# Optimization experiments

Hardware: AMD Instinct MI355X
Metric: run time of the kernel (lower is better)

The kernel has to match this reference:

```python
import jax, jax.numpy as jnp
import numpy as np

D_MODEL = 2048
N_HEADS = 16
N_KV = 4
D_HEAD = D_MODEL // N_HEADS  # 128
KERNEL = 4
TOTAL_QKV = (N_HEADS + 2 * N_KV) * D_HEAD  # 3072
BATCH, SEQ = 2, 2048


def setup_inputs() -> dict:
    key = jax.random.key(0)
    ks = jax.random.split(key, 6)
    s = 1.0 / np.sqrt(D_MODEL)
    return {
        "hidden_states": jax.random.normal(ks[0], (BATCH, SEQ, D_MODEL), jnp.float32),
        "w_q": jax.random.normal(ks[1], (D_MODEL, N_HEADS * D_HEAD), jnp.float32) * s,
        "w_k": jax.random.normal(ks[2], (D_MODEL, N_KV * D_HEAD), jnp.float32) * s,
        "w_v": jax.random.normal(ks[3], (D_MODEL, N_KV * D_HEAD), jnp.float32) * s,
        "w_o": jax.random.normal(ks[4], (N_HEADS * D_HEAD, D_MODEL), jnp.float32) * s,
        "conv_w": jax.random.normal(ks[5], (TOTAL_QKV, KERNEL), jnp.float32) * 0.1,
    }


def _canon_b(x, conv_w):
    """Depthwise causal conv1d with residual. x: [B,S,C], conv_w: [C,K]."""
    K = conv_w.shape[1]
    xp = jnp.pad(x, ((0, 0), (K - 1, 0), (0, 0)))  # left pad for causality
    S = x.shape[1]
    out = sum(xp[:, k:k + S, :] * conv_w[:, k] for k in range(K))
    return x + out


def reference(hidden_states, w_q, w_k, w_v, w_o, conv_w):
    B, S, _ = hidden_states.shape
    q = hidden_states @ w_q   # [B,S,Hq*Dh]
    k = hidden_states @ w_k   # [B,S,Hkv*Dh]
    v = hidden_states @ w_v
    qkv = jnp.concatenate([q, k, v], axis=-1)
    qkv = _canon_b(qkv, conv_w)
    q_dim = N_HEADS * D_HEAD
    kv_dim = N_KV * D_HEAD
    q, k, v = jnp.split(qkv, [q_dim, q_dim + kv_dim], axis=-1)
    q = q.reshape(B, S, N_HEADS, D_HEAD)
    k = k.reshape(B, S, N_KV, D_HEAD)
    v = v.reshape(B, S, N_KV, D_HEAD)
    # GQA: repeat kv heads to match query heads
    groups = N_HEADS // N_KV
    k = jnp.repeat(k, groups, axis=2)
    v = jnp.repeat(v, groups, axis=2)
    scale = 1.0 / np.sqrt(D_HEAD)
    scores = jnp.einsum("bqhd,bkhd->bhqk", q, k) * scale  # [B,H,S,S]
    causal = jnp.tril(jnp.ones((S, S), dtype=bool))
    scores = jnp.where(causal, scores, jnp.finfo(scores.dtype).min)
    probs = jax.nn.softmax(scores, axis=-1)
    attended = jnp.einsum("bhqk,bkhd->bqhd", probs, v)  # [B,S,H,Dh]
    attended = attended.reshape(B, S, N_HEADS * D_HEAD)
    return attended @ w_o
```

## Files before the change

### kernel.cpp

```cpp
#include <hip/hip_runtime.h>
#include <stdint.h>

typedef unsigned short u16;
typedef short short8 __attribute__((ext_vector_type(8)));
typedef float f32x4 __attribute__((ext_vector_type(4)));
typedef float f32x16 __attribute__((ext_vector_type(16)));

#define DM    2048
#define NH    16
#define NKV   4
#define DH    128
#define TQKV  3072
#define NB    2
#define SEQL  2048
#define MROWS (NB * SEQL)
#define QDIM  (NH * DH)
#define KVDIM (NKV * DH)
#define QSCALE 0.08838834764831845f

#define MFMA16(a, b, c) __builtin_amdgcn_mfma_f32_16x16x32_bf16((a), (b), (c), 0, 0, 0)
#define MFMA32(a, b, c) __builtin_amdgcn_mfma_f32_32x32x16_bf16((a), (b), (c), 0, 0, 0)

__device__ __forceinline__ u16 f2bf(float f) {
  uint32_t u = __float_as_uint(f);
  u += 0x7fffu + ((u >> 16) & 1u);
  return (u16)(u >> 16);
}
__device__ __forceinline__ float bf2f(u16 h) {
  return __uint_as_float(((uint32_t)h) << 16);
}
__device__ __forceinline__ void gload16(const u16* g, u16* l) {
  __builtin_amdgcn_global_load_lds((__attribute__((address_space(1))) void*)(u16*)g,
                                   (__attribute__((address_space(3))) void*)l, 16, 0, 0);
}
__device__ __forceinline__ uint32_t cvtpk(float lo, float hi) {
  uint32_t r;
  asm("v_cvt_pk_bf16_f32 %0, %1, %2" : "=v"(r) : "v"(lo), "v"(hi));
  return r;
}
__device__ __forceinline__ void swapln(uint32_t& a, uint32_t& b) {
  asm volatile("v_permlane32_swap_b32 %0, %1" : "+v"(a), "+v"(b));
}

__global__ void k_f32_to_bf16(const float* __restrict__ src, u16* __restrict__ dst, int n) {
  int i = (blockIdx.x * blockDim.x + threadIdx.x) * 4;
  if (i >= n) return;
  float4 v = *reinterpret_cast<const float4*>(src + i);
  u16 o0 = f2bf(v.x), o1 = f2bf(v.y), o2 = f2bf(v.z), o3 = f2bf(v.w);
  u16* d = dst + i;
  d[0] = o0; d[1] = o1; d[2] = o2; d[3] = o3;
}

__global__ void k_transpose_f32_bf16(const float* __restrict__ src, u16* __restrict__ dst,
                                     int K, int N, int rowOff, int dstLd) {
  __shared__ float t[32][33];
  const int n0 = blockIdx.x * 32, k0 = blockIdx.y * 32;
  const int tx = threadIdx.x, ty = threadIdx.y;
#pragma unroll
  for (int i = ty; i < 32; i += 8)
    t[i][tx] = src[(size_t)(k0 + i) * N + (n0 + tx)];
  __syncthreads();
#pragma unroll
  for (int i = ty; i < 32; i += 8)
    dst[(size_t)(rowOff + n0 + i) * dstLd + (k0 + tx)] = f2bf(t[tx][i]);
}

__global__ void k_transpose_bf16(const u16* __restrict__ src, u16* __restrict__ dst, int R, int C) {
  __shared__ u16 t[32][33];
  const size_t zoff = (size_t)blockIdx.z * R * C;
  const int c0 = blockIdx.x * 32, r0 = blockIdx.y * 32;
  const int tx = threadIdx.x, ty = threadIdx.y;
#pragma unroll
  for (int i = ty; i < 32; i += 8)
    t[i][tx] = src[zoff + (size_t)(r0 + i) * C + (c0 + tx)];
  __syncthreads();
#pragma unroll
  for (int i = ty; i < 32; i += 8)
    dst[zoff + (size_t)(c0 + i) * R + (r0 + tx)] = t[tx][i];
}

template <int OUTBF>
__global__ __launch_bounds__(256) void k_gemm_bt(const u16* __restrict__ A, const u16* __restrict__ Bt,
                                                 float* __restrict__ Cf, u16* __restrict__ Cb,
                                                 int M, int N, int K) {
  __shared__ u16 As[2][128 * 32];
  __shared__ u16 Bs[2][128 * 32];
  const int tid = threadIdx.x;
  const int m0 = blockIdx.x * 128;
  const int n0 = blockIdx.y * 128;
  const int r  = tid >> 2;
  const int c8 = (tid & 3) << 3;
  const u16* Ag0 = A  + (size_t)(m0 + r) * K + c8;
  const u16* Ag1 = A  + (size_t)(m0 + 64 + r) * K + c8;
  const u16* Bg0 = Bt + (size_t)(n0 + r) * K + c8;
  const u16* Bg1 = Bt + (size_t)(n0 + 64 + r) * K + c8;

  auto stage = [&](int buf, int kt) {
    const int kg = kt * 32;
    gload16(Ag0 + kg, &As[buf][tid * 8]);
    gload16(Ag1 + kg, &As[buf][2048 + tid * 8]);
    gload16(Bg0 + kg, &Bs[buf][tid * 8]);
    gload16(Bg1 + kg, &Bs[buf][2048 + tid * 8]);
  };

  f32x4 acc[4][4];
#pragma unroll
  for (int i = 0; i < 4; ++i)
#pragma unroll
    for (int j = 0; j < 4; ++j) acc[i][j] = (f32x4){0.f, 0.f, 0.f, 0.f};

  const int wv = tid >> 6, ln = tid & 63;
  const int wr = (wv >> 1) * 64, wc = (wv & 1) * 64;
  const int lr = ln & 15, lko = (ln >> 4) * 8;

  stage(0, 0);
  __syncthreads();

  const int nk = K >> 5;
  for (int kt = 0; kt < nk; ++kt) {
    const int cur = kt & 1;
    if (kt + 1 < nk) stage(cur ^ 1, kt + 1);
    short8 af[4], bf[4];
#pragma unroll
    for (int i = 0; i < 4; ++i)
      af[i] = *reinterpret_cast<const short8*>(&As[cur][(wr + i * 16 + lr) * 32 + lko]);
#pragma unroll
    for (int i = 0; i < 4; ++i)
      bf[i] = *reinterpret_cast<const short8*>(&Bs[cur][(wc + i * 16 + lr) * 32 + lko]);
#pragma unroll
    for (int i = 0; i < 4; ++i)
#pragma unroll
      for (int j = 0; j < 4; ++j)
        acc[i][j] = MFMA16(af[i], bf[j], acc[i][j]);
    __syncthreads();
  }

  const int rg = (ln >> 4) * 4;
#pragma unroll
  for (int i = 0; i < 4; ++i) {
#pragma unroll
    for (int j = 0; j < 4; ++j) {
      const int row = m0 + wr + i * 16 + rg;
      const int col = n0 + wc + j * 16 + lr;
#pragma unroll
      for (int q = 0; q < 4; ++q) {
        float v = acc[i][j][q];
        if (OUTBF) Cb[(size_t)(row + q) * N + col] = f2bf(v);
        else       Cf[(size_t)(row + q) * N + col] = v;
      }
    }
  }
}

__global__ void k_conv_route(const u16* __restrict__ qkv, const float* __restrict__ cw,
                             u16* __restrict__ Qh, u16* __restrict__ Kh, u16* __restrict__ Vsd) {
  const int row = blockIdx.x;
  const int b = row >> 11, s = row & 2047;
  const int c = threadIdx.x * 8;
  float x[4][8];
#pragma unroll
  for (int k = 0; k < 4; ++k) {
    const int sr = s + k - 3;
    if (sr < 0) {
#pragma unroll
      for (int j = 0; j < 8; ++j) x[k][j] = 0.f;
    } else {
      short8 v = *reinterpret_cast<const short8*>(&qkv[(size_t)(b * SEQL + sr) * TQKV + c]);
#pragma unroll
      for (int j = 0; j < 8; ++j) x[k][j] = bf2f((u16)v[j]);
    }
  }
  float o[8];
#pragma unroll
  for (int j = 0; j < 8; ++j) {
    float4 w4 = *reinterpret_cast<const float4*>(&cw[(c + j) * 4]);
    o[j] = x[3][j] + x[0][j] * w4.x + x[1][j] * w4.y + x[2][j] * w4.z + x[3][j] * w4.w;
  }
  short8 ov;
  if (c < QDIM) {
#pragma unroll
    for (int j = 0; j < 8; ++j) ov[j] = (short)f2bf(o[j] * QSCALE);
    const int h = c >> 7, d = c & 127;
    *reinterpret_cast<short8*>(&Qh[((size_t)(b * NH + h) * SEQL + s) * DH + d]) = ov;
  } else if (c < QDIM + KVDIM) {
#pragma unroll
    for (int j = 0; j < 8; ++j) ov[j] = (short)f2bf(o[j]);
    const int cc = c - QDIM;
    const int h = cc >> 7, d = cc & 127;
    *reinterpret_cast<short8*>(&Kh[((size_t)(b * NKV + h) * SEQL + s) * DH + d]) = ov;
  } else {
#pragma unroll
    for (int j = 0; j < 8; ++j) ov[j] = (short)f2bf(o[j]);
    const int cc = c - QDIM - KVDIM;
    const int h = cc >> 7, d = cc & 127;
    *reinterpret_cast<short8*>(&Vsd[((size_t)(b * NKV + h) * SEQL + s) * DH + d]) = ov;
  }
}

__global__ __launch_bounds__(512) void k_attn(const u16* __restrict__ Qh, const u16* __restrict__ Kh,
                                              const u16* __restrict__ Vt, u16* __restrict__ att) {
  __shared__ u16 Ks[2][64 * 128];
  __shared__ u16 Vs[2][128 * 64];
  const int qb = blockIdx.x, h = blockIdx.y, b = blockIdx.z;
  const int kvh = h >> 2;
  const int tid = threadIdx.x, wv = tid >> 6, ln = tid & 63;
  const int lq = ln & 31, hi = ln >> 5;
  const int hi16 = hi * 16;
  const int q0w = qb * 256 + wv * 32;
  const int qg = q0w + lq;
  const int swr = (lq & 7) << 4;

  const u16* qrow = Qh + ((size_t)(b * NH + h) * SEQL + qg) * DH;
  short8 qf[8];
#pragma unroll
  for (int dblk = 0; dblk < 8; ++dblk)
    qf[dblk] = *reinterpret_cast<const short8*>(qrow + dblk * 16 + hi * 8);

  const u16* kg = Kh + (size_t)(b * NKV + kvh) * SEQL * DH;
  const u16* vg = Vt + (size_t)(b * NKV + kvh) * DH * SEQL;

  const int ck0 = tid, ck1 = tid + 512;
  const int krow0 = ck0 >> 4, kcb0 = (ck0 & 15) << 4;
  const int krow1 = ck1 >> 4, kcb1 = (ck1 & 15) << 4;
  const int koff0 = krow0 * DH + ((kcb0 ^ ((krow0 & 7) << 4)) >> 1);
  const int koff1 = krow1 * DH + ((kcb1 ^ ((krow1 & 7) << 4)) >> 1);
  const int vd0 = ck0 >> 3, vcb0 = (ck0 & 7) << 4;
  const int vd1 = ck1 >> 3, vcb1 = (ck1 & 7) << 4;
  const int voff0 = vd0 * SEQL + ((vcb0 ^ ((vd0 & 7) << 4)) >> 1);
  const int voff1 = vd1 * SEQL + ((vcb1 ^ ((vd1 & 7) << 4)) >> 1);

  auto stage = [&](int buf, int kvs) {
    gload16(kg + (size_t)kvs * DH + koff0, &Ks[buf][ck0 * 8]);
    gload16(kg + (size_t)kvs * DH + koff1, &Ks[buf][ck1 * 8]);
    gload16(vg + (size_t)kvs + voff0, &Vs[buf][ck0 * 8]);
    gload16(vg + (size_t)kvs + voff1, &Vs[buf][ck1 * 8]);
  };

  f32x16 oacc[4];
#pragma unroll
  for (int nb = 0; nb < 4; ++nb)
#pragma unroll
    for (int r = 0; r < 16; ++r) oacc[nb][r] = 0.f;
  float mrow = -1e30f, lrow = 0.f;

  const int ntiles = (qb + 1) * 4;
  stage(0, 0);
  __syncthreads();

  for (int t = 0; t < ntiles; ++t) {
    const int cur = t & 1;
    const int kvs = t * 64;
    if (t + 1 < ntiles) stage(cur ^ 1, kvs + 64);
    if (kvs <= q0w + 31) {
      const u16* ks = Ks[cur];
      const u16* vs = Vs[cur];
      f32x16 st[2];
#pragma unroll
      for (int kvb = 0; kvb < 2; ++kvb)
#pragma unroll
        for (int r = 0; r < 16; ++r) st[kvb][r] = 0.f;

      __builtin_amdgcn_s_setprio(1);
#pragma unroll
      for (int kvb = 0; kvb < 2; ++kvb) {
        const u16* krow = ks + (kvb * 32 + lq) * 128;
#pragma unroll
        for (int dblk = 0; dblk < 8; ++dblk) {
          short8 kf = *reinterpret_cast<const short8*>(krow + (((dblk * 32 + hi16) ^ swr) >> 1));
          st[kvb] = MFMA32(kf, qf[dblk], st[kvb]);
        }
      }
      __builtin_amdgcn_s_setprio(0);

      if (kvs + 63 > q0w) {
#pragma unroll
        for (int kvb = 0; kvb < 2; ++kvb)
#pragma unroll
          for (int r = 0; r < 16; ++r) {
            const int kvg = kvs + kvb * 32 + (r & 3) + 8 * (r >> 2) + 4 * hi;
            if (kvg > qg) st[kvb][r] = -1e30f;
          }
      }

      float tm = st[0][0];
#pragma unroll
      for (int kvb = 0; kvb < 2; ++kvb)
#pragma unroll
        for (int r = 0; r < 16; ++r) tm = fmaxf(tm, st[kvb][r]);
      tm = fmaxf(tm, __shfl_xor(tm, 32));
      if (__any(tm > mrow + 8.f)) {
        const float nm = fmaxf(mrow, tm);
        const float scl = __expf(mrow - nm);
        mrow = nm;
        lrow *= scl;
#pragma unroll
        for (int nb = 0; nb < 4; ++nb)
#pragma unroll
          for (int r = 0; r < 16; ++r) oacc[nb][r] *= scl;
      }
      float ps = 0.f;
#pragma unroll
      for (int kvb = 0; kvb < 2; ++kvb)
#pragma unroll
        for (int r = 0; r < 16; ++r) {
          const float p = __expf(st[kvb][r] - mrow);
          st[kvb][r] = p;
          ps += p;
        }
      ps += __shfl_xor(ps, 32);
      lrow += ps;

      uint32_t w[4][4];
#pragma unroll
      for (int kvb = 0; kvb < 2; ++kvb) {
        uint32_t x0 = cvtpk(st[kvb][0], st[kvb][1]);
        uint32_t y0 = cvtpk(st[kvb][4], st[kvb][5]);
        swapln(x0, y0);
        uint32_t x1 = cvtpk(st[kvb][2], st[kvb][3]);
        uint32_t y1 = cvtpk(st[kvb][6], st[kvb][7]);
        swapln(x1, y1);
        w[kvb * 2][0] = x0; w[kvb * 2][1] = x1; w[kvb * 2][2] = y0; w[kvb * 2][3] = y1;
        uint32_t x2 = cvtpk(st[kvb][8], st[kvb][9]);
        uint32_t y2 = cvtpk(st[kvb][12], st[kvb][13]);
        swapln(x2, y2);
        uint32_t x3 = cvtpk(st[kvb][10], st[kvb][11]);
        uint32_t y3 = cvtpk(st[kvb][14], st[kvb][15]);
        swapln(x3, y3);
        w[kvb * 2 + 1][0] = x2; w[kvb * 2 + 1][1] = x3; w[kvb * 2 + 1][2] = y2; w[kvb * 2 + 1][3] = y3;
      }
      short8 pa[4];
#pragma unroll
      for (int kc = 0; kc < 4; ++kc) {
        union { uint32_t uw[4]; short8 s; } pu;
#pragma unroll
        for (int j = 0; j < 4; ++j) pu.uw[j] = w[kc][j];
        pa[kc] = pu.s;
      }

      __builtin_amdgcn_s_setprio(1);
#pragma unroll
      for (int nb = 0; nb < 4; ++nb) {
        const u16* vrow = vs + (nb * 32 + lq) * 64;
#pragma unroll
        for (int kc = 0; kc < 4; ++kc) {
          short8 vf = *reinterpret_cast<const short8*>(vrow + (((kc * 32 + hi16) ^ swr) >> 1));
          oacc[nb] = MFMA32(vf, pa[kc], oacc[nb]);
        }
      }
      __builtin_amdgcn_s_setprio(0);
    }
    __syncthreads();
  }

  const float inv = 1.0f / lrow;
  u16* orow = att + ((size_t)(b * SEQL + qg)) * QDIM + h * DH;
#pragma unroll
  for (int nb = 0; nb < 4; ++nb)
#pragma unroll
    for (int rg = 0; rg < 4; ++rg) {
      const int r = rg * 4;
      uint2 vout;
      vout.x = cvtpk(oacc[nb][r] * inv, oacc[nb][r + 1] * inv);
      vout.y = cvtpk(oacc[nb][r + 2] * inv, oacc[nb][r + 3] * inv);
      *reinterpret_cast<uint2*>(orow + nb * 32 + 8 * rg + 4 * hi) = vout;
    }
}

extern "C" void kernel_launch(void* const* d_in, const int* in_sizes, int n_in,
                              void* d_out, int out_size, void* d_ws, size_t ws_size,
                              hipStream_t stream) {
  const float* hin = (const float*)d_in[0];
  const float* wq  = (const float*)d_in[1];
  const float* wk  = (const float*)d_in[2];
  const float* wvv = (const float*)d_in[3];
  const float* wo  = (const float*)d_in[4];
  const float* cw  = (const float*)d_in[5];
  float* out = (float*)d_out;
  char* ws = (char*)d_ws;

  u16* h_bf = (u16*)(ws + 0);
  u16* Wt   = (u16*)(ws + 16777216);
  u16* Wot  = (u16*)(ws + 29360128);
  u16* Qh   = (u16*)(ws + 37748736);
  u16* Kh   = (u16*)(ws + 54525952);
  u16* Vsd  = (u16*)(ws + 58720256);
  u16* Vt   = (u16*)(ws + 62914560);
  u16* att  = (u16*)(ws + 67108864);
  u16* qkv  = (u16*)d_out;

  dim3 tb(32, 8);
  k_f32_to_bf16<<<8192, 256, 0, stream>>>(hin, h_bf, MROWS * DM);
  k_transpose_f32_bf16<<<dim3(64, 64), tb, 0, stream>>>(wq, Wt, 2048, 2048, 0, 2048);
  k_transpose_f32_bf16<<<dim3(16, 64), tb, 0, stream>>>(wk, Wt, 2048, 512, 2048, 2048);
  k_transpose_f32_bf16<<<dim3(16, 64), tb, 0, stream>>>(wvv, Wt, 2048, 512, 2560, 2048);
  k_transpose_f32_bf16<<<dim3(64, 64), tb, 0, stream>>>(wo, Wot, 2048, 2048, 0, 2048);
  k_gemm_bt<1><<<dim3(32, 24), 256, 0, stream>>>(h_bf, Wt, nullptr, qkv, MROWS, TQKV, DM);
  k_conv_route<<<MROWS, 384, 0, stream>>>(qkv, cw, Qh, Kh, Vsd);
  k_transpose_bf16<<<dim3(4, 64, NB * NKV), tb, 0, stream>>>(Vsd, Vt, SEQL, DH);
  k_attn<<<dim3(SEQL / 256, NH, NB), 512, 0, stream>>>(Qh, Kh, Vt, att);
  k_gemm_bt<0><<<dim3(32, 16), 256, 0, stream>>>(att, Wot, out, nullptr, MROWS, DM, DM);
}
```

Measured before the change: 251.8 us.

## Shrink attention blocks to 128 queries with balanced 1D grid and exp2 softmax

Attention blocks now cover 128 queries with 4 waves instead of 256 with 8. The launch is a flat 512-block grid whose query-block order is reversed for batch 0, so heavy causal blocks get scheduled early and load balance improves. The log2(e) factor is folded into the Q scale so the softmax can use exp2. The max and sum reductions are split into four independent chains for more ILP, and the lazy rescale threshold is raised to match base-2 units. The cost is that each K/V tile is loaded by twice as many blocks, so total global and LDS traffic rises.

```diff
diff --git a/kernel.cpp b/kernel.cpp
--- a/kernel.cpp
+++ b/kernel.cpp
@@ -16,7 +16,7 @@
 #define MROWS (NB * SEQL)
 #define QDIM  (NH * DH)
 #define KVDIM (NKV * DH)
-#define QSCALE 0.08838834764831845f
+#define QSCALE_L2E 0.1275174336f
 
 #define MFMA16(a, b, c) __builtin_amdgcn_mfma_f32_16x16x32_bf16((a), (b), (c), 0, 0, 0)
 #define MFMA32(a, b, c) __builtin_amdgcn_mfma_f32_32x32x16_bf16((a), (b), (c), 0, 0, 0)
@@ -179,7 +179,7 @@
   short8 ov;
   if (c < QDIM) {
 #pragma unroll
-    for (int j = 0; j < 8; ++j) ov[j] = (short)f2bf(o[j] * QSCALE);
+    for (int j = 0; j < 8; ++j) ov[j] = (short)f2bf(o[j] * QSCALE_L2E);
     const int h = c >> 7, d = c & 127;
     *reinterpret_cast<short8*>(&Qh[((size_t)(b * NH + h) * SEQL + s) * DH + d]) = ov;
   } else if (c < QDIM + KVDIM) {
@@ -197,16 +197,20 @@
   }
 }
 
-__global__ __launch_bounds__(512) void k_attn(const u16* __restrict__ Qh, const u16* __restrict__ Kh,
+__global__ __launch_bounds__(256) void k_attn(const u16* __restrict__ Qh, const u16* __restrict__ Kh,
                                               const u16* __restrict__ Vt, u16* __restrict__ att) {
   __shared__ u16 Ks[2][64 * 128];
   __shared__ u16 Vs[2][128 * 64];
-  const int qb = blockIdx.x, h = blockIdx.y, b = blockIdx.z;
+  const int L = blockIdx.x;
+  const int b = L >> 8;
+  const int r255 = L & 255;
+  const int h = r255 >> 4;
+  const int qi = b ? (r255 & 15) : 15 - (r255 & 15);
   const int kvh = h >> 2;
   const int tid = threadIdx.x, wv = tid >> 6, ln = tid & 63;
   const int lq = ln & 31, hi = ln >> 5;
   const int hi16 = hi * 16;
-  const int q0w = qb * 256 + wv * 32;
+  const int q0w = qi * 128 + wv * 32;
   const int qg = q0w + lq;
   const int swr = (lq & 7) << 4;
 
@@ -219,21 +223,23 @@
   const u16* kg = Kh + (size_t)(b * NKV + kvh) * SEQL * DH;
   const u16* vg = Vt + (size_t)(b * NKV + kvh) * DH * SEQL;
 
-  const int ck0 = tid, ck1 = tid + 512;
-  const int krow0 = ck0 >> 4, kcb0 = (ck0 & 15) << 4;
-  const int krow1 = ck1 >> 4, kcb1 = (ck1 & 15) << 4;
-  const int koff0 = krow0 * DH + ((kcb0 ^ ((krow0 & 7) << 4)) >> 1);
-  const int koff1 = krow1 * DH + ((kcb1 ^ ((krow1 & 7) << 4)) >> 1);
-  const int vd0 = ck0 >> 3, vcb0 = (ck0 & 7) << 4;
-  const int vd1 = ck1 >> 3, vcb1 = (ck1 & 7) << 4;
-  const int voff0 = vd0 * SEQL + ((vcb0 ^ ((vd0 & 7) << 4)) >> 1);
-  const int voff1 = vd1 * SEQL + ((vcb1 ^ ((vd1 & 7) << 4)) >> 1);
+  int koff[4], voff[4];
+#pragma unroll
+  for (int j = 0; j < 4; ++j) {
+    const int ck = tid + j * 256;
+    const int krow = ck >> 4, kcb = (ck & 15) << 4;
+    koff[j] = krow * DH + ((kcb ^ ((krow & 7) << 4)) >> 1);
+    const int vd = ck >> 3, vcb = (ck & 7) << 4;
+    voff[j] = vd * SEQL + ((vcb ^ ((vd & 7) << 4)) >> 1);
+  }
 
   auto stage = [&](int buf, int kvs) {
-    gload16(kg + (size_t)kvs * DH + koff0, &Ks[buf][ck0 * 8]);
-    gload16(kg + (size_t)kvs * DH + koff1, &Ks[buf][ck1 * 8]);
-    gload16(vg + (size_t)kvs + voff0, &Vs[buf][ck0 * 8]);
-    gload16(vg + (size_t)kvs + voff1, &Vs[buf][ck1 * 8]);
+#pragma unroll
+    for (int j = 0; j < 4; ++j)
+      gload16(kg + (size_t)kvs * DH + koff[j], &Ks[buf][(tid + j * 256) * 8]);
+#pragma unroll
+    for (int j = 0; j < 4; ++j)
+      gload16(vg + (size_t)kvs + voff[j], &Vs[buf][(tid + j * 256) * 8]);
   };
 
   f32x16 oacc[4];
@@ -243,7 +249,7 @@
     for (int r = 0; r < 16; ++r) oacc[nb][r] = 0.f;
   float mrow = -1e30f, lrow = 0.f;
 
-  const int ntiles = (qb + 1) * 4;
+  const int ntiles = qi * 2 + 2;
   stage(0, 0);
   __syncthreads();
 
@@ -282,15 +288,21 @@
           }
       }
 
-      float tm = st[0][0];
+      float a0 = st[0][0], a1 = st[0][1], a2 = st[0][2], a3 = st[0][3];
 #pragma unroll
       for (int kvb = 0; kvb < 2; ++kvb)
 #pragma unroll
-        for (int r = 0; r < 16; ++r) tm = fmaxf(tm, st[kvb][r]);
+        for (int r = (kvb ? 0 : 4); r < 16; r += 4) {
+          a0 = fmaxf(a0, st[kvb][r]);
+          a1 = fmaxf(a1, st[kvb][r + 1]);
+          a2 = fmaxf(a2, st[kvb][r + 2]);
+          a3 = fmaxf(a3, st[kvb][r + 3]);
+        }
+      float tm = fmaxf(fmaxf(a0, a1), fmaxf(a2, a3));
       tm = fmaxf(tm, __shfl_xor(tm, 32));
-      if (__any(tm > mrow + 8.f)) {
+      if (__any(tm > mrow + 11.0f)) {
         const float nm = fmaxf(mrow, tm);
-        const float scl = __expf(mrow - nm);
+        const float scl = exp2f(mrow - nm);
         mrow = nm;
         lrow *= scl;
 #pragma unroll
@@ -298,15 +310,19 @@
 #pragma unroll
           for (int r = 0; r < 16; ++r) oacc[nb][r] *= scl;
       }
-      float ps = 0.f;
+      float s0 = 0.f, s1 = 0.f, s2 = 0.f, s3 = 0.f;
 #pragma unroll
       for (int kvb = 0; kvb < 2; ++kvb)
 #pragma unroll
-        for (int r = 0; r < 16; ++r) {
-          const float p = __expf(st[kvb][r] - mrow);
-          st[kvb][r] = p;
-          ps += p;
+        for (int r = 0; r < 16; r += 4) {
+          float p0 = exp2f(st[kvb][r] - mrow);
+          float p1 = exp2f(st[kvb][r + 1] - mrow);
+          float p2 = exp2f(st[kvb][r + 2] - mrow);
+          float p3 = exp2f(st[kvb][r + 3] - mrow);
+          st[kvb][r] = p0; st[kvb][r + 1] = p1; st[kvb][r + 2] = p2; st[kvb][r + 3] = p3;
+          s0 += p0; s1 += p1; s2 += p2; s3 += p3;
         }
+      float ps = (s0 + s1) + (s2 + s3);
       ps += __shfl_xor(ps, 32);
       lrow += ps;
 
@@ -397,6 +413,6 @@
   k_gemm_bt<1><<<dim3(32, 24), 256, 0, stream>>>(h_bf, Wt, nullptr, qkv, MROWS, TQKV, DM);
   k_conv_route<<<MROWS, 384, 0, stream>>>(qkv, cw, Qh, Kh, Vsd);
   k_transpose_bf16<<<dim3(4, 64, NB * NKV), tb, 0, stream>>>(Vsd, Vt, SEQL, DH);
-  k_attn<<<dim3(SEQL / 256, NH, NB), 512, 0, stream>>>(Qh, Kh, Vt, att);
+  k_attn<<<dim3(512), 256, 0, stream>>>(Qh, Kh, Vt, att);
   k_gemm_bt<0><<<dim3(32, 16), 256, 0, stream>>>(att, Wot, out, nullptr, MROWS, DM, DM);
 }
```

Measured after the change: 290.8 us. 15.5% more time.
